# Performance work log

Measured on AMD Instinct MI355X. Metric: run time of the kernel, lower is better.

Reference implementation:

```python
import jax, jax.numpy as jnp
import numpy as np

B, S, E, HD = 32, 1024, 768, 64


def _rope_tables(seq_len, dim):
    # theta = 10000 ** (-2*arange(0,dim,2)/dim); freqs = pos * theta
    theta = jnp.power(10000.0, -2.0 * jnp.arange(0, dim, 2, dtype=jnp.float32) / dim)
    pos = jnp.arange(seq_len, dtype=jnp.float32)[:, None]          # [S,1]
    freqs = pos * theta[None, :]                                    # [S,dim//2]
    cos = jnp.repeat(jnp.cos(freqs), 2, axis=-1)                    # [S,dim]
    sin = jnp.repeat(jnp.sin(freqs), 2, axis=-1)                    # [S,dim]
    return cos, sin


def _apply_rope(x, cos, sin):
    # rotate-half interleaved: new[...,0::2] = -x[...,1::2]; new[...,1::2] = x[...,0::2]
    b, s, d = x.shape
    x2 = x.reshape(b, s, d // 2, 2)
    rot = jnp.stack([-x2[..., 1], x2[..., 0]], axis=-1).reshape(b, s, d)
    return x * cos[None] + rot * sin[None]


def setup_inputs() -> dict:
    key = jax.random.key(0)
    k0, k1, k2, k3 = jax.random.split(key, 4)
    x = jax.random.normal(k0, (B, S, E), dtype=jnp.float32)
    Wq = jax.random.normal(k1, (HD, E), dtype=jnp.float32) * 0.02
    Wk = jax.random.normal(k2, (HD, E), dtype=jnp.float32) * 0.02
    Wv = jax.random.normal(k3, (HD, E), dtype=jnp.float32) * 0.02
    return {"x": x, "Wq": Wq, "Wk": Wk, "Wv": Wv}


def reference(x, Wq, Wk, Wv):
    b, s, e = x.shape
    q = jnp.einsum('bse,he->bsh', x, Wq)
    k = jnp.einsum('bse,he->bsh', x, Wk)
    v = jnp.einsum('bse,he->bsh', x, Wv)
    cos, sin = _rope_tables(s, q.shape[-1])
    rq = _apply_rope(q, cos, sin)
    rk = _apply_rope(k, cos, sin)
    scale = e ** (-0.5)  # NOTE: original scales by emb_dim, not head_size
    scores = jnp.einsum('bqh,bkh->bqk', rq, rk) * scale
    causal = jnp.tril(jnp.ones((s, s), dtype=bool))
    scores = jnp.where(causal[None], scores, -jnp.inf)
    attn = jax.nn.softmax(scores, axis=-1)
    return jnp.einsum('bqk,bkh->bqh', attn, v)
```

## Files before the change

### kernel.cpp

```cpp
#include <hip/hip_runtime.h>
#include <hip/hip_bf16.h>

#define B_  32
#define S_  1024
#define E_  768
#define HD_ 64
#define M_  (B_*S_)

typedef __attribute__((ext_vector_type(8))) short short8;
typedef __attribute__((ext_vector_type(4))) float float4v;

__device__ __forceinline__ float bf2f(unsigned short u) {
    union { unsigned int i; float f; } c; c.i = ((unsigned int)u) << 16; return c.f;
}
__device__ __forceinline__ unsigned short f2bf(float x) {
    union { float f; unsigned u; } c; c.f = x;
    unsigned r = (c.u + 0x7FFFu + ((c.u >> 16) & 1u)) >> 16;
    return (unsigned short)r;
}

__device__ __forceinline__ void gld_lds16(const void* g, void* l) {
    __builtin_amdgcn_global_load_lds(
        (const __attribute__((address_space(1))) unsigned int*)g,
        (__attribute__((address_space(3))) unsigned int*)l,
        16, 0, 0);
}

__global__ __launch_bounds__(256) void setup_kernel(const unsigned int* __restrict__ xw,
                                                    unsigned int* __restrict__ flag,
                                                    float* __restrict__ cs_t,
                                                    float* __restrict__ sn_t) {
    if (blockIdx.x == 128) {
        __shared__ int cnt;
        if (threadIdx.x == 0) cnt = 0;
        __syncthreads();
        unsigned int w = xw[(size_t)threadIdx.x * 33331];
        unsigned int e = (w >> 8) & 0x7F;
        int hit = (e >= 0x3B && e <= 0x40) ? 1 : 0;
        atomicAdd(&cnt, hit);
        __syncthreads();
        if (threadIdx.x == 0) *flag = (cnt > 128) ? 1u : 0u;
        return;
    }
    int idx = blockIdx.x * 256 + threadIdx.x;
    int pos = idx >> 5;
    int ii  = idx & 31;
    float theta = exp2f(-(float)ii * 0.8304820237218406f);
    float fr = (float)pos * theta;
    float sn, cs;
    sincosf(fr, &sn, &cs);
    cs_t[idx] = cs;
    sn_t[idx] = sn;
}

__global__ __launch_bounds__(512, 4) void qkv_mfma_kernel(
    const void* __restrict__ x_, const void* __restrict__ Wq_,
    const void* __restrict__ Wk_, const void* __restrict__ Wv_,
    const unsigned int* __restrict__ flag,
    const float* __restrict__ cs_t, const float* __restrict__ sn_t,
    unsigned short* __restrict__ rq, unsigned short* __restrict__ rk,
    unsigned short* __restrict__ vt)
{
    __shared__ __align__(16) unsigned short smem[2][32 * 512];

    const bool isb = (*flag != 0);
    const int t    = threadIdx.x;
    const int lane = t & 63;
    const int wave = t >> 6;
    const int quad = lane >> 4;
    const int l15  = lane & 15;
    const int row0 = blockIdx.x * 64;
    const int h    = wave >> 2;
    const int cw   = wave & 3;

    const void* gbase[4];
    unsigned    eo[4];
    int         tidv[4];
    #pragma unroll
    for (int i = 0; i < 4; ++i) {
        int tid = wave * 4 + i;
        tidv[i] = tid;
        if (tid < 8) {
            int gmt = tid >> 1, ks = tid & 1;
            gbase[i] = x_;
            eo[i] = (unsigned)((row0 + gmt * 16 + l15) * E_ + ks * 32 + quad * 8);
        } else {
            int bi = tid - 8, ct = bi >> 1, ks = bi & 1;
            int reg = ct >> 2;
            gbase[i] = (reg == 0) ? Wq_ : (reg == 1 ? Wk_ : Wv_);
            eo[i] = (unsigned)(((ct & 3) * 16 + l15) * E_ + ks * 32 + quad * 8);
        }
    }

    float4v acc[3][2];
    #pragma unroll
    for (int nt = 0; nt < 3; ++nt)
        #pragma unroll
        for (int mtl = 0; mtl < 2; ++mtl)
            #pragma unroll
            for (int r = 0; r < 4; ++r) acc[nt][mtl][r] = 0.f;

    auto stage = [&](int k0, int bsel) {
        if (isb) {
            #pragma unroll
            for (int i = 0; i < 4; ++i)
                gld_lds16((const unsigned short*)gbase[i] + eo[i] + k0,
                          &smem[bsel][(size_t)tidv[i] * 512]);
        } else {
            #pragma unroll
            for (int i = 0; i < 4; ++i) {
                const float* f = (const float*)gbase[i] + eo[i] + k0;
                float4 a = *(const float4*)f, bq = *(const float4*)(f + 4);
                uint4 w;
                w.x = f2bf(a.x)  | ((unsigned)f2bf(a.y)  << 16);
                w.y = f2bf(a.z)  | ((unsigned)f2bf(a.w)  << 16);
                w.z = f2bf(bq.x) | ((unsigned)f2bf(bq.y) << 16);
                w.w = f2bf(bq.z) | ((unsigned)f2bf(bq.w) << 16);
                *(uint4*)(&smem[bsel][(size_t)tidv[i] * 512] + (size_t)lane * 8) = w;
            }
        }
    };

    stage(0, 0);
    int buf = 0;
    for (int c = 0; c < 12; ++c) {
        __syncthreads();
        if (c < 11) stage((c + 1) * 64, buf ^ 1);
        const unsigned short* sb = smem[buf];
        #pragma unroll
        for (int ks = 0; ks < 2; ++ks) {
            short8 af[2];
            #pragma unroll
            for (int mtl = 0; mtl < 2; ++mtl)
                af[mtl] = *(const short8*)(sb + (size_t)((h * 2 + mtl) * 2 + ks) * 512 + lane * 8);
            #pragma unroll
            for (int nt = 0; nt < 3; ++nt) {
                int ct = cw * 3 + nt;
                short8 bf = *(const short8*)(sb + (size_t)(8 + ct * 2 + ks) * 512 + lane * 8);
                #pragma unroll
                for (int mtl = 0; mtl < 2; ++mtl)
                    acc[nt][mtl] = __builtin_amdgcn_mfma_f32_16x16x32_bf16(
                        af[mtl], bf, acc[nt][mtl], 0, 0, 0);
            }
        }
        buf ^= 1;
    }

    const int b      = row0 >> 10;
    const int s_in_b = row0 & (S_ - 1);
    #pragma unroll
    for (int nt = 0; nt < 3; ++nt) {
        int ct = cw * 3 + nt;
        int c0 = ct * 16;
        int region = c0 >> 6;
        int d = (c0 & 63) + l15;
        if (region < 2) {
            unsigned short* dst = (region == 0) ? rq : rk;
            int ii = d >> 1;
            #pragma unroll
            for (int mtl = 0; mtl < 2; ++mtl) {
                #pragma unroll
                for (int r = 0; r < 4; ++r) {
                    int row = row0 + (h * 2 + mtl) * 16 + quad * 4 + r;
                    int pos = row & (S_ - 1);
                    float cs = cs_t[pos * 32 + ii];
                    float sn = sn_t[pos * 32 + ii];
                    float val = acc[nt][mtl][r];
                    float partner = __shfl_xor(val, 1);
                    float res = (d & 1) ? fmaf(val, cs,  partner * sn)
                                        : fmaf(val, cs, -partner * sn);
                    dst[(size_t)row * HD_ + d] = f2bf(res);
                }
            }
        } else {
            #pragma unroll
            for (int mtl = 0; mtl < 2; ++mtl) {
                int sb2 = s_in_b + (h * 2 + mtl) * 16 + quad * 4;
                ushort4 pk;
                pk.x = f2bf(acc[nt][mtl][0]);
                pk.y = f2bf(acc[nt][mtl][1]);
                pk.z = f2bf(acc[nt][mtl][2]);
                pk.w = f2bf(acc[nt][mtl][3]);
                *(ushort4*)(vt + ((size_t)(b * 64 + d) * S_ + sb2)) = pk;
            }
        }
    }
}

__global__ __launch_bounds__(256, 2) void attn_mfma_kernel(
    const unsigned short* __restrict__ rq, const unsigned short* __restrict__ rk,
    const unsigned short* __restrict__ vt, const unsigned int* __restrict__ flag,
    void* __restrict__ out)
{
    __shared__ __align__(16) unsigned short kv[2][32 * 512];
    __shared__ unsigned short plds[4][16][72];

    const bool isb = (*flag != 0);
    const int t    = threadIdx.x;
    const int lane = t & 63;
    const int wave = t >> 6;
    const int quad = lane >> 4;
    const int l15  = lane & 15;
    const int qt   = blockIdx.x;
    const int b    = blockIdx.y;
    const int q0   = qt * 64 + wave * 16;
    const float scale = 0.03608439182435161f;

    const unsigned short* qp = rq + ((size_t)(b * S_ + q0 + l15)) * HD_ + quad * 8;
    short8 qf0 = *(const short8*)qp;
    short8 qf1 = *(const short8*)(qp + 32);

    const unsigned short* sbase[8];
    unsigned eo[8];
    int      slotv[8], tidv[8], stride[8];
    #pragma unroll
    for (int i = 0; i < 8; ++i) {
        int tid = wave * 8 + i;
        tidv[i] = tid;
        int isV  = tid >> 4;
        int rem  = tid & 15;
        int slot = rem >> 3;
        int wi   = rem & 7;
        int nt   = wi >> 1, ks = wi & 1;
        slotv[i] = slot;
        if (!isV) {
            sbase[i]  = rk;
            eo[i]     = (unsigned)((b * S_ + nt * 16 + l15) * HD_ + ks * 32 + quad * 8);
            stride[i] = 64 * HD_;
        } else {
            sbase[i]  = vt;
            eo[i]     = (unsigned)((b * 64 + nt * 16 + l15) * S_ + ks * 32 + quad * 8);
            stride[i] = 64;
        }
    }

    float4v o[4];
    float m_[4], l_[4];
    #pragma unroll
    for (int nt = 0; nt < 4; ++nt)
        #pragma unroll
        for (int r = 0; r < 4; ++r) o[nt][r] = 0.f;
    #pragma unroll
    for (int r = 0; r < 4; ++r) { m_[r] = -1e30f; l_[r] = 0.f; }

    const int nIter = (qt + 2) >> 1;

    auto stage = [&](int it, int bsel) {
        int ta  = 2 * it;
        int tb  = min(ta + 1, qt);
        #pragma unroll
        for (int i = 0; i < 8; ++i) {
            int kt = slotv[i] ? tb : ta;
            gld_lds16(sbase[i] + eo[i] + (size_t)kt * stride[i],
                      &kv[bsel][(size_t)tidv[i] * 512]);
        }
    };

    stage(0, 0);
    int buf = 0;
    for (int i = 0; i < nIter; ++i) {
        __syncthreads();
        if (i + 1 < nIter) stage(i + 1, buf ^ 1);
        const unsigned short* kb = kv[buf];

        float sc[2][4][4];
        #pragma unroll
        for (int slot = 0; slot < 2; ++slot) {
            #pragma unroll
            for (int nt = 0; nt < 4; ++nt) {
                float4v s;
                #pragma unroll
                for (int r = 0; r < 4; ++r) s[r] = 0.f;
                short8 kf0 = *(const short8*)(kb + (size_t)(slot * 8 + nt * 2 + 0) * 512 + lane * 8);
                short8 kf1 = *(const short8*)(kb + (size_t)(slot * 8 + nt * 2 + 1) * 512 + lane * 8);
                s = __builtin_amdgcn_mfma_f32_16x16x32_bf16(qf0, kf0, s, 0, 0, 0);
                s = __builtin_amdgcn_mfma_f32_16x16x32_bf16(qf1, kf1, s, 0, 0, 0);
                #pragma unroll
                for (int r = 0; r < 4; ++r) sc[slot][nt][r] = s[r] * scale;
            }
        }

        if (2 * i + 1 >= qt) {
            #pragma unroll
            for (int slot = 0; slot < 2; ++slot) {
                int ktl = 2 * i + slot;
                #pragma unroll
                for (int nt = 0; nt < 4; ++nt) {
                    int kg = ktl * 64 + nt * 16 + l15;
                    #pragma unroll
                    for (int r = 0; r < 4; ++r) {
                        int qg = q0 + quad * 4 + r;
                        if (kg > qg) sc[slot][nt][r] = -1e30f;
                    }
                }
            }
        }

        float mx[4];
        #pragma unroll
        for (int r = 0; r < 4; ++r) {
            float a0 = fmaxf(fmaxf(sc[0][0][r], sc[0][1][r]), fmaxf(sc[0][2][r], sc[0][3][r]));
            float a1 = fmaxf(fmaxf(sc[1][0][r], sc[1][1][r]), fmaxf(sc[1][2][r], sc[1][3][r]));
            mx[r] = fmaxf(a0, a1);
        }
        #pragma unroll
        for (int st = 1; st < 16; st <<= 1)
            #pragma unroll
            for (int r = 0; r < 4; ++r)
                mx[r] = fmaxf(mx[r], __shfl_xor(mx[r], st));

        float al[4];
        #pragma unroll
        for (int r = 0; r < 4; ++r) {
            float mn = fmaxf(m_[r], mx[r]);
            al[r] = __expf(m_[r] - mn);
            m_[r] = mn;
        }

        float sm[4] = {0.f, 0.f, 0.f, 0.f};
        #pragma unroll
        for (int slot = 0; slot < 2; ++slot)
            #pragma unroll
            for (int nt = 0; nt < 4; ++nt)
                #pragma unroll
                for (int r = 0; r < 4; ++r) {
                    float p = __expf(sc[slot][nt][r] - m_[r]);
                    sc[slot][nt][r] = p;
                    sm[r] += p;
                }
        #pragma unroll
        for (int st = 1; st < 16; st <<= 1)
            #pragma unroll
            for (int r = 0; r < 4; ++r)
                sm[r] += __shfl_xor(sm[r], st);
        #pragma unroll
        for (int r = 0; r < 4; ++r) l_[r] = l_[r] * al[r] + sm[r];

        #pragma unroll
        for (int nt = 0; nt < 4; ++nt)
            #pragma unroll
            for (int r = 0; r < 4; ++r) o[nt][r] *= al[r];

        #pragma unroll
        for (int slot = 0; slot < 2; ++slot) {
            #pragma unroll
            for (int nt = 0; nt < 4; ++nt)
                #pragma unroll
                for (int r = 0; r < 4; ++r)
                    plds[wave][quad * 4 + r][nt * 16 + l15] = f2bf(sc[slot][nt][r]);
            short8 pf0 = *(const short8*)&plds[wave][l15][quad * 8];
            short8 pf1 = *(const short8*)&plds[wave][l15][32 + quad * 8];
            #pragma unroll
            for (int nt = 0; nt < 4; ++nt) {
                short8 vf0 = *(const short8*)(kb + (size_t)(16 + slot * 8 + nt * 2 + 0) * 512 + lane * 8);
                short8 vf1 = *(const short8*)(kb + (size_t)(16 + slot * 8 + nt * 2 + 1) * 512 + lane * 8);
                o[nt] = __builtin_amdgcn_mfma_f32_16x16x32_bf16(pf0, vf0, o[nt], 0, 0, 0);
                o[nt] = __builtin_amdgcn_mfma_f32_16x16x32_bf16(pf1, vf1, o[nt], 0, 0, 0);
            }
        }
        buf ^= 1;
    }

    float inv[4];
    #pragma unroll
    for (int r = 0; r < 4; ++r) inv[r] = 1.0f / l_[r];
    if (isb) {
        unsigned short* op = (unsigned short*)out;
        #pragma unroll
        for (int nt = 0; nt < 4; ++nt)
            #pragma unroll
            for (int r = 0; r < 4; ++r) {
                size_t row = (size_t)b * S_ + q0 + quad * 4 + r;
                op[row * HD_ + nt * 16 + l15] = f2bf(o[nt][r] * inv[r]);
            }
    } else {
        float* op = (float*)out;
        #pragma unroll
        for (int nt = 0; nt < 4; ++nt)
            #pragma unroll
            for (int r = 0; r < 4; ++r) {
                size_t row = (size_t)b * S_ + q0 + quad * 4 + r;
                op[row * HD_ + nt * 16 + l15] = o[nt][r] * inv[r];
            }
    }
}

extern "C" void kernel_launch(void* const* d_in, const int* in_sizes, int n_in,
                              void* d_out, int out_size, void* d_ws, size_t ws_size,
                              hipStream_t stream) {
    const void* x  = d_in[0];
    const void* Wq = d_in[1];
    const void* Wk = d_in[2];
    const void* Wv = d_in[3];

    unsigned int* flag = (unsigned int*)d_ws;
    float* cs_t = (float*)d_ws + 64;
    float* sn_t = cs_t + (size_t)S_ * 32;
    unsigned short* rq = (unsigned short*)(sn_t + (size_t)S_ * 32);
    unsigned short* rk = rq + (size_t)M_ * HD_;
    unsigned short* vt = rk + (size_t)M_ * HD_;

    hipLaunchKernelGGL(setup_kernel, dim3(129), dim3(256), 0, stream,
                       (const unsigned int*)x, flag, cs_t, sn_t);
    hipLaunchKernelGGL(qkv_mfma_kernel, dim3(M_ / 64), dim3(512), 0, stream,
                       x, Wq, Wk, Wv, flag, cs_t, sn_t, rq, rk, vt);
    hipLaunchKernelGGL(attn_mfma_kernel, dim3(S_ / 64, B_), dim3(256), 0, stream,
                       rq, rk, vt, flag, d_out);
}
```

Baseline: 219.6 us.

## Pre-pack weights and Q/K/V tiles into MFMA fragment layout, stage full x row-block

Adds a small kernel that converts and packs Wq/Wk/Wv into MFMA fragment-order tiles once. The QKV projection now loads its entire 64x768 x block into swizzled LDS up front and streams only the packed weight tiles through a double buffer. Q, K and V are written in a tiled fragment-contiguous layout so the attention kernel can load them with a uniform contiguous stride. This is meant to cut global/LDS address overhead, redundant weight conversion and strided K/V fetches. The trade-off is much larger LDS use, which lowers occupancy to 2 blocks, plus an extra kernel launch.

```diff
diff --git a/kernel.cpp b/kernel.cpp
--- a/kernel.cpp
+++ b/kernel.cpp
@@ -10,9 +10,6 @@
 typedef __attribute__((ext_vector_type(8))) short short8;
 typedef __attribute__((ext_vector_type(4))) float float4v;
 
-__device__ __forceinline__ float bf2f(unsigned short u) {
-    union { unsigned int i; float f; } c; c.i = ((unsigned int)u) << 16; return c.f;
-}
 __device__ __forceinline__ unsigned short f2bf(float x) {
     union { float f; unsigned u; } c; c.f = x;
     unsigned r = (c.u + 0x7FFFu + ((c.u >> 16) & 1u)) >> 16;
@@ -53,15 +50,45 @@
     sn_t[idx] = sn;
 }
 
-__global__ __launch_bounds__(512, 4) void qkv_mfma_kernel(
-    const void* __restrict__ x_, const void* __restrict__ Wq_,
-    const void* __restrict__ Wk_, const void* __restrict__ Wv_,
+__global__ __launch_bounds__(256) void wpack_kernel(
+    const void* __restrict__ Wq_, const void* __restrict__ Wk_,
+    const void* __restrict__ Wv_, const unsigned int* __restrict__ flag,
+    unsigned short* __restrict__ wp)
+{
+    const bool isb = (*flag != 0);
+    int gid  = blockIdx.x * 256 + threadIdx.x;
+    int lane = gid & 63;
+    int tIdx = gid >> 6;
+    int ct   = tIdx / 24;
+    int rem  = tIdx - ct * 24;
+    int c    = rem >> 1, ks = rem & 1;
+    int quad = lane >> 4, l15 = lane & 15;
+    const void* wsel = (ct < 4) ? Wq_ : (ct < 8 ? Wk_ : Wv_);
+    int row = (ct & 3) * 16 + l15;
+    int col = c * 64 + ks * 32 + quad * 8;
+    uint4 w;
+    if (isb) {
+        w = *(const uint4*)((const unsigned short*)wsel + (size_t)row * E_ + col);
+    } else {
+        const float* f = (const float*)wsel + (size_t)row * E_ + col;
+        float4 a = *(const float4*)f, bq = *(const float4*)(f + 4);
+        w.x = f2bf(a.x)  | ((unsigned)f2bf(a.y)  << 16);
+        w.y = f2bf(a.z)  | ((unsigned)f2bf(a.w)  << 16);
+        w.z = f2bf(bq.x) | ((unsigned)f2bf(bq.y) << 16);
+        w.w = f2bf(bq.z) | ((unsigned)f2bf(bq.w) << 16);
+    }
+    *(uint4*)(wp + (size_t)gid * 8) = w;
+}
+
+__global__ __launch_bounds__(512, 2) void qkv_mfma_kernel(
+    const void* __restrict__ x_, const unsigned short* __restrict__ wp,
     const unsigned int* __restrict__ flag,
     const float* __restrict__ cs_t, const float* __restrict__ sn_t,
-    unsigned short* __restrict__ rq, unsigned short* __restrict__ rk,
-    unsigned short* __restrict__ vt)
+    unsigned short* __restrict__ rq_p, unsigned short* __restrict__ rk_p,
+    unsigned short* __restrict__ vt_p)
 {
-    __shared__ __align__(16) unsigned short smem[2][32 * 512];
+    __shared__ __align__(16) unsigned short Alds[64 * 768];
+    __shared__ __align__(16) unsigned short Blds[2][24 * 512];
 
     const bool isb = (*flag != 0);
     const int t    = threadIdx.x;
@@ -73,23 +100,26 @@
     const int h    = wave >> 2;
     const int cw   = wave & 3;
 
-    const void* gbase[4];
-    unsigned    eo[4];
-    int         tidv[4];
-    #pragma unroll
-    for (int i = 0; i < 4; ++i) {
-        int tid = wave * 4 + i;
-        tidv[i] = tid;
-        if (tid < 8) {
-            int gmt = tid >> 1, ks = tid & 1;
-            gbase[i] = x_;
-            eo[i] = (unsigned)((row0 + gmt * 16 + l15) * E_ + ks * 32 + quad * 8);
-        } else {
-            int bi = tid - 8, ct = bi >> 1, ks = bi & 1;
-            int reg = ct >> 2;
-            gbase[i] = (reg == 0) ? Wq_ : (reg == 1 ? Wk_ : Wv_);
-            eo[i] = (unsigned)(((ct & 3) * 16 + l15) * E_ + ks * 32 + quad * 8);
-        }
+    unsigned eoA[12];
+    unsigned ldsA[12];
+    #pragma unroll
+    for (int j = 0; j < 12; ++j) {
+        unsigned L    = (unsigned)(wave * 12 + j) * 1024u + (unsigned)lane * 16u;
+        unsigned row  = L / 1536u;
+        unsigned colb = L - row * 1536u;
+        unsigned win  = colb >> 7, off = colb & 127u;
+        unsigned gcol = (win << 7) | (off ^ ((row & 7u) << 4));
+        eoA[j]  = row * 768u + (gcol >> 1);
+        ldsA[j] = (unsigned)(wave * 12 + j) * 1024u;
+    }
+
+    unsigned aA[2][2];
+    #pragma unroll
+    for (int mtl = 0; mtl < 2; ++mtl) {
+        unsigned rl = (unsigned)((h * 2 + mtl) * 16 + l15);
+        #pragma unroll
+        for (int ks = 0; ks < 2; ++ks)
+            aA[mtl][ks] = rl * 1536u + 16u * ((((unsigned)ks << 2) | (unsigned)quad) ^ (rl & 7u));
     }
 
     float4v acc[3][2];
@@ -100,49 +130,55 @@
             #pragma unroll
             for (int r = 0; r < 4; ++r) acc[nt][mtl][r] = 0.f;
 
-    auto stage = [&](int k0, int bsel) {
-        if (isb) {
-            #pragma unroll
-            for (int i = 0; i < 4; ++i)
-                gld_lds16((const unsigned short*)gbase[i] + eo[i] + k0,
-                          &smem[bsel][(size_t)tidv[i] * 512]);
-        } else {
-            #pragma unroll
-            for (int i = 0; i < 4; ++i) {
-                const float* f = (const float*)gbase[i] + eo[i] + k0;
-                float4 a = *(const float4*)f, bq = *(const float4*)(f + 4);
-                uint4 w;
-                w.x = f2bf(a.x)  | ((unsigned)f2bf(a.y)  << 16);
-                w.y = f2bf(a.z)  | ((unsigned)f2bf(a.w)  << 16);
-                w.z = f2bf(bq.x) | ((unsigned)f2bf(bq.y) << 16);
-                w.w = f2bf(bq.z) | ((unsigned)f2bf(bq.w) << 16);
-                *(uint4*)(&smem[bsel][(size_t)tidv[i] * 512] + (size_t)lane * 8) = w;
-            }
+    auto stageB = [&](int c, int bsel) {
+        #pragma unroll
+        for (int i = 0; i < 3; ++i) {
+            int idx = wave * 3 + i;
+            int ct = idx >> 1, ks = idx & 1;
+            gld_lds16(wp + ((size_t)((ct * 12 + c) * 2 + ks)) * 512 + lane * 8,
+                      &Blds[bsel][(size_t)idx * 512]);
         }
     };
 
-    stage(0, 0);
+    if (isb) {
+        const unsigned short* xb = (const unsigned short*)x_ + (size_t)row0 * E_;
+        #pragma unroll
+        for (int j = 0; j < 12; ++j)
+            gld_lds16(xb + eoA[j], (char*)Alds + ldsA[j]);
+    } else {
+        const float* xb = (const float*)x_ + (size_t)row0 * E_;
+        #pragma unroll
+        for (int j = 0; j < 12; ++j) {
+            const float* f = xb + eoA[j];
+            float4 a = *(const float4*)f, bq = *(const float4*)(f + 4);
+            uint4 w;
+            w.x = f2bf(a.x)  | ((unsigned)f2bf(a.y)  << 16);
+            w.y = f2bf(a.z)  | ((unsigned)f2bf(a.w)  << 16);
+            w.z = f2bf(bq.x) | ((unsigned)f2bf(bq.y) << 16);
+            w.w = f2bf(bq.z) | ((unsigned)f2bf(bq.w) << 16);
+            *(uint4*)((char*)Alds + ldsA[j] + (size_t)lane * 16) = w;
+        }
+    }
+    stageB(0, 0);
+    __syncthreads();
+
     int buf = 0;
     for (int c = 0; c < 12; ++c) {
-        __syncthreads();
-        if (c < 11) stage((c + 1) * 64, buf ^ 1);
-        const unsigned short* sb = smem[buf];
+        if (c < 11) stageB(c + 1, buf ^ 1);
         #pragma unroll
         for (int ks = 0; ks < 2; ++ks) {
             short8 af[2];
-            #pragma unroll
-            for (int mtl = 0; mtl < 2; ++mtl)
-                af[mtl] = *(const short8*)(sb + (size_t)((h * 2 + mtl) * 2 + ks) * 512 + lane * 8);
+            af[0] = *(const short8*)((const char*)Alds + aA[0][ks] + c * 128);
+            af[1] = *(const short8*)((const char*)Alds + aA[1][ks] + c * 128);
             #pragma unroll
             for (int nt = 0; nt < 3; ++nt) {
                 int ct = cw * 3 + nt;
-                short8 bf = *(const short8*)(sb + (size_t)(8 + ct * 2 + ks) * 512 + lane * 8);
-                #pragma unroll
-                for (int mtl = 0; mtl < 2; ++mtl)
-                    acc[nt][mtl] = __builtin_amdgcn_mfma_f32_16x16x32_bf16(
-                        af[mtl], bf, acc[nt][mtl], 0, 0, 0);
-            }
-        }
+                short8 bf = *(const short8*)(&Blds[buf][(size_t)(ct * 2 + ks) * 512 + lane * 8]);
+                acc[nt][0] = __builtin_amdgcn_mfma_f32_16x16x32_bf16(af[0], bf, acc[nt][0], 0, 0, 0);
+                acc[nt][1] = __builtin_amdgcn_mfma_f32_16x16x32_bf16(af[1], bf, acc[nt][1], 0, 0, 0);
+            }
+        }
+        __syncthreads();
         buf ^= 1;
     }
 
@@ -151,12 +187,12 @@
     #pragma unroll
     for (int nt = 0; nt < 3; ++nt) {
         int ct = cw * 3 + nt;
-        int c0 = ct * 16;
-        int region = c0 >> 6;
-        int d = (c0 & 63) + l15;
+        int region = ct >> 2;
+        int d = (ct & 3) * 16 + l15;
         if (region < 2) {
-            unsigned short* dst = (region == 0) ? rq : rk;
+            unsigned short* dst = (region == 0) ? rq_p : rk_p;
             int ii = d >> 1;
+            int ksq = d >> 5, quadq = (d >> 3) & 3, e = d & 7;
             #pragma unroll
             for (int mtl = 0; mtl < 2; ++mtl) {
                 #pragma unroll
@@ -169,27 +205,34 @@
                     float partner = __shfl_xor(val, 1);
                     float res = (d & 1) ? fmaf(val, cs,  partner * sn)
                                         : fmaf(val, cs, -partner * sn);
-                    dst[(size_t)row * HD_ + d] = f2bf(res);
+                    int kt = pos >> 6, ntq = (pos >> 4) & 3, l15q = pos & 15;
+                    size_t idx = ((((size_t)(b * 16 + kt) * 4 + ntq) * 2 + ksq) * 64
+                                  + quadq * 16 + l15q) * 8 + e;
+                    dst[idx] = f2bf(res);
                 }
             }
         } else {
+            int ntv = ct & 3;
             #pragma unroll
             for (int mtl = 0; mtl < 2; ++mtl) {
                 int sb2 = s_in_b + (h * 2 + mtl) * 16 + quad * 4;
+                int kt = sb2 >> 6, ksv = (sb2 >> 5) & 1, quadv = (sb2 >> 3) & 3, e0 = sb2 & 7;
                 ushort4 pk;
                 pk.x = f2bf(acc[nt][mtl][0]);
                 pk.y = f2bf(acc[nt][mtl][1]);
                 pk.z = f2bf(acc[nt][mtl][2]);
                 pk.w = f2bf(acc[nt][mtl][3]);
-                *(ushort4*)(vt + ((size_t)(b * 64 + d) * S_ + sb2)) = pk;
+                size_t idx = ((((size_t)(b * 16 + kt) * 4 + ntv) * 2 + ksv) * 64
+                              + quadv * 16 + l15) * 8 + e0;
+                *(ushort4*)(vt_p + idx) = pk;
             }
         }
     }
 }
 
 __global__ __launch_bounds__(256, 2) void attn_mfma_kernel(
-    const unsigned short* __restrict__ rq, const unsigned short* __restrict__ rk,
-    const unsigned short* __restrict__ vt, const unsigned int* __restrict__ flag,
+    const unsigned short* __restrict__ rq_p, const unsigned short* __restrict__ rk_p,
+    const unsigned short* __restrict__ vt_p, const unsigned int* __restrict__ flag,
     void* __restrict__ out)
 {
     __shared__ __align__(16) unsigned short kv[2][32 * 512];
@@ -206,13 +249,13 @@
     const int q0   = qt * 64 + wave * 16;
     const float scale = 0.03608439182435161f;
 
-    const unsigned short* qp = rq + ((size_t)(b * S_ + q0 + l15)) * HD_ + quad * 8;
-    short8 qf0 = *(const short8*)qp;
-    short8 qf1 = *(const short8*)(qp + 32);
+    const unsigned short* qb = rq_p + ((size_t)((b * 16 + qt) * 4 + wave) * 2) * 512;
+    short8 qf0 = *(const short8*)(qb + lane * 8);
+    short8 qf1 = *(const short8*)(qb + 512 + lane * 8);
 
     const unsigned short* sbase[8];
     unsigned eo[8];
-    int      slotv[8], tidv[8], stride[8];
+    int      slotv[8], tidv[8];
     #pragma unroll
     for (int i = 0; i < 8; ++i) {
         int tid = wave * 8 + i;
@@ -223,15 +266,8 @@
         int wi   = rem & 7;
         int nt   = wi >> 1, ks = wi & 1;
         slotv[i] = slot;
-        if (!isV) {
-            sbase[i]  = rk;
-            eo[i]     = (unsigned)((b * S_ + nt * 16 + l15) * HD_ + ks * 32 + quad * 8);
-            stride[i] = 64 * HD_;
-        } else {
-            sbase[i]  = vt;
-            eo[i]     = (unsigned)((b * 64 + nt * 16 + l15) * S_ + ks * 32 + quad * 8);
-            stride[i] = 64;
-        }
+        sbase[i] = isV ? vt_p : rk_p;
+        eo[i]    = (unsigned)(((b * 64 + nt) * 2 + ks) * 512 + lane * 8);
     }
 
     float4v o[4];
@@ -251,7 +287,7 @@
         #pragma unroll
         for (int i = 0; i < 8; ++i) {
             int kt = slotv[i] ? tb : ta;
-            gld_lds16(sbase[i] + eo[i] + (size_t)kt * stride[i],
+            gld_lds16(sbase[i] + eo[i] + (size_t)kt * 4096,
                       &kv[bsel][(size_t)tidv[i] * 512]);
         }
     };
@@ -396,14 +432,17 @@
     unsigned int* flag = (unsigned int*)d_ws;
     float* cs_t = (float*)d_ws + 64;
     float* sn_t = cs_t + (size_t)S_ * 32;
-    unsigned short* rq = (unsigned short*)(sn_t + (size_t)S_ * 32);
-    unsigned short* rk = rq + (size_t)M_ * HD_;
-    unsigned short* vt = rk + (size_t)M_ * HD_;
+    unsigned short* wp   = (unsigned short*)(sn_t + (size_t)S_ * 32);
+    unsigned short* rq_p = wp + (size_t)288 * 512;
+    unsigned short* rk_p = rq_p + (size_t)M_ * HD_;
+    unsigned short* vt_p = rk_p + (size_t)M_ * HD_;
 
     hipLaunchKernelGGL(setup_kernel, dim3(129), dim3(256), 0, stream,
                        (const unsigned int*)x, flag, cs_t, sn_t);
+    hipLaunchKernelGGL(wpack_kernel, dim3(72), dim3(256), 0, stream,
+                       Wq, Wk, Wv, flag, wp);
     hipLaunchKernelGGL(qkv_mfma_kernel, dim3(M_ / 64), dim3(512), 0, stream,
-                       x, Wq, Wk, Wv, flag, cs_t, sn_t, rq, rk, vt);
+                       x, wp, flag, cs_t, sn_t, rq_p, rk_p, vt_p);
     hipLaunchKernelGGL(attn_mfma_kernel, dim3(S_ / 64, B_), dim3(256), 0, stream,
-                       rq, rk, vt, flag, d_out);
-}
+                       rq_p, rk_p, vt_p, flag, d_out);
+}
```

Result: faster. 207.5 us (-5.5%).
